# Kernel optimization log

Hardware: AMD Instinct MI355X
Metric: run time of the kernel (lower is better)

The kernel has to match this reference:

```python
import jax, jax.numpy as jnp
import numpy as np

DIM = 64          # hidden dim
EDGE_DIM = 6      # edge feature dim
A = 6             # action_dim (torsion bins); also torsions per graph
B = 512           # num_graphs
NPG = 40          # nodes per graph
N = B * NPG       # 20480 nodes
E = 43008         # edges
T = B * A         # 3072 total torsions


def _lin_init(k, out_f, in_f):
    bound = 1.0 / np.sqrt(in_f)
    kw, kb = jax.random.split(k)
    w = jax.random.uniform(kw, (out_f, in_f), jnp.float32, -bound, bound)
    b = jax.random.uniform(kb, (out_f,), jnp.float32, -bound, bound)
    return w, b


def setup_inputs() -> dict:
    key = jax.random.key(0)
    ks = jax.random.split(key, 24)
    inp = {}
    inp['x'] = jax.random.normal(ks[0], (N, 3), jnp.float32)
    inp['edge_attr'] = jax.random.uniform(ks[1], (E, EDGE_DIM), jnp.float32)
    inp['edge_index'] = jax.random.randint(ks[2], (2, E), 0, N)
    inp['batch'] = jnp.arange(N, dtype=jnp.int32) // NPG            # graph-sorted
    inp['nrbidx'] = jnp.repeat(jnp.arange(B, dtype=jnp.int32), A)   # torsion -> graph
    inp['nonring'] = jax.random.randint(ks[3], (T, 4), 0, N)        # 4 atoms per torsion
    # parameters
    inp['lin0_w'], inp['lin0_b'] = _lin_init(ks[4], DIM, 3)
    inp['enn1_w'], inp['enn1_b'] = _lin_init(ks[5], DIM, EDGE_DIM)
    inp['enn2_w'], inp['enn2_b'] = _lin_init(ks[6], DIM * DIM, DIM)
    inp['root_w'] = jax.random.uniform(ks[7], (DIM, DIM), jnp.float32, -1/np.sqrt(DIM), 1/np.sqrt(DIM))
    inp['conv_b'] = jnp.zeros((DIM,), jnp.float32)
    inp['gru_w_ih'], inp['gru_b_ih'] = _lin_init(ks[8], 3 * DIM, DIM)
    inp['gru_w_hh'], inp['gru_b_hh'] = _lin_init(ks[9], 3 * DIM, DIM)
    inp['s2s_w_ih'], inp['s2s_b_ih'] = _lin_init(ks[10], 4 * DIM, 2 * DIM)
    inp['s2s_w_hh'], inp['s2s_b_hh'] = _lin_init(ks[11], 4 * DIM, DIM)
    inp['mem_w_ih'], inp['mem_b_ih'] = _lin_init(ks[12], 4 * DIM, 2 * DIM)
    inp['mem_w_hh'], inp['mem_b_hh'] = _lin_init(ks[13], 4 * DIM, DIM)
    inp['lin1_w'], inp['lin1_b'] = _lin_init(ks[14], DIM, 5 * DIM)
    inp['lin2_w'], inp['lin2_b'] = _lin_init(ks[15], A, DIM)
    return inp


def _lstm_cell(xin, hc, w_ih, w_hh, b_ih, b_hh):
    h, c = hc
    g = xin @ w_ih.T + b_ih + h @ w_hh.T + b_hh
    i, f, gg, o = jnp.split(g, 4, axis=-1)
    c2 = jax.nn.sigmoid(f) * c + jax.nn.sigmoid(i) * jnp.tanh(gg)
    h2 = jax.nn.sigmoid(o) * jnp.tanh(c2)
    return h2, (h2, c2)


def reference(x, edge_attr, lin0_w, lin0_b, enn1_w, enn1_b, enn2_w, enn2_b,
              root_w, conv_b, gru_w_ih, gru_b_ih, gru_w_hh, gru_b_hh,
              s2s_w_ih, s2s_b_ih, s2s_w_hh, s2s_b_hh,
              mem_w_ih, mem_b_ih, mem_w_hh, mem_b_hh,
              lin1_w, lin1_b, lin2_w, lin2_b,
              edge_index, batch, nrbidx, nonring):
    dim = DIM
    out = jax.nn.relu(x @ lin0_w.T + lin0_b)                         # (N, dim)
    # edge-conditioned weights (constant across the 6 iterations)
    ew = jax.nn.relu(edge_attr @ enn1_w.T + enn1_b)
    W = (ew @ enn2_w.T + enn2_b).reshape(-1, dim, dim)               # (E, dim, dim)
    src, dst = edge_index[0], edge_index[1]
    deg = jax.ops.segment_sum(jnp.ones_like(src, jnp.float32), dst, num_segments=N)
    denom = jnp.maximum(deg, 1.0)[:, None]
    h = out                                                          # GRU hidden
    for _ in range(6):
        msg = jnp.einsum('ei,eio->eo', out[src], W)                  # gather + bmm
        agg = jax.ops.segment_sum(msg, dst, num_segments=N) / denom  # scatter-mean
        m = jax.nn.relu(agg + out @ root_w + conv_b)                 # NNConv out
        gi = m @ gru_w_ih.T + gru_b_ih
        gh = h @ gru_w_hh.T + gru_b_hh
        ir, iz, inn = jnp.split(gi, 3, axis=-1)
        hr, hz, hn = jnp.split(gh, 3, axis=-1)
        r = jax.nn.sigmoid(ir + hr)
        z = jax.nn.sigmoid(iz + hz)
        n = jnp.tanh(inn + r * hn)
        h = (1.0 - z) * n + z * h
        out = h
    # Set2Set pooling (processing_steps=6)
    q_star = jnp.zeros((B, 2 * dim), out.dtype)
    hc = (jnp.zeros((B, dim), out.dtype), jnp.zeros((B, dim), out.dtype))
    for _ in range(6):
        q, hc = _lstm_cell(q_star, hc, s2s_w_ih, s2s_w_hh, s2s_b_ih, s2s_b_hh)
        e = jnp.sum(out * q[batch], axis=-1)                         # (N,)
        emax = jax.ops.segment_max(e, batch, num_segments=B)
        a = jnp.exp(e - emax[batch])
        a = a / jax.ops.segment_sum(a, batch, num_segments=B)[batch]
        r = jax.ops.segment_sum(a[:, None] * out, batch, num_segments=B)
        q_star = jnp.concatenate([q, r], axis=-1)                    # (B, 2*dim)
    # memory LSTM, one step, zero initial state
    hc0 = (jnp.zeros((B, dim), out.dtype), jnp.zeros((B, dim), out.dtype))
    lstm_out, (hx, cx) = _lstm_cell(q_star, hc0, mem_w_ih, mem_w_hh, mem_b_ih, mem_b_hh)
    t = lstm_out[nrbidx].reshape(B, 1, A, dim)
    nd = out[nonring.reshape(-1)].reshape(B, 4, A, dim)
    z2 = jnp.concatenate([t, nd], axis=1)                            # (B, 5, A, dim)
    z2 = jnp.transpose(z2, (0, 3, 2, 1)).reshape(-1, 5 * dim)        # (T, 5*dim)
    z2 = jax.nn.relu(z2 @ lin1_w.T + lin1_b)
    z2 = z2 @ lin2_w.T + lin2_b                                      # (T, A)
    logit = z2.reshape(B, A, A)   # equal torsion counts -> pad_sequence == reshape
    return (logit, hx[None], cx[None])
```

## Files before the change

kernel.cpp:

```cpp
#include <hip/hip_runtime.h>
#include <hip/hip_fp16.h>

#define NN 20480
#define EE 43008
#define BB 512
#define TT 3072

typedef _Float16 f16;
typedef _Float16 f16x8 __attribute__((ext_vector_type(8)));
typedef float f32x4 __attribute__((ext_vector_type(4)));

__device__ __forceinline__ float sigm(float x) { return 1.0f / (1.0f + __expf(-x)); }
__device__ __forceinline__ float tanh_f(float x) {
    float xc = fminf(fmaxf(x, -15.f), 15.f);
    float t = __expf(2.f * xc);
    return (t - 1.f) / (t + 1.f);
}

__global__ void k_prep0(const float* __restrict__ x, const float* __restrict__ ea,
                        const float* __restrict__ l0w, const float* __restrict__ l0b,
                        const float* __restrict__ e1w, const float* __restrict__ e1b,
                        const float* __restrict__ e2w, const float* __restrict__ e2b,
                        const float* __restrict__ rootw,
                        const float* __restrict__ gwih, const float* __restrict__ gwhh,
                        const float* __restrict__ swih, const float* __restrict__ swhh,
                        const float* __restrict__ mwih,
                        float* __restrict__ feat, f16* __restrict__ feat16, f16* __restrict__ ew16,
                        f16* __restrict__ qmtp, float* __restrict__ deg,
                        f16* __restrict__ rootp, f16* __restrict__ wihp, f16* __restrict__ whhp,
                        float* __restrict__ s2sihT, float* __restrict__ s2shhT,
                        float* __restrict__ memihT)
{
    const int S0 = NN;
    const int S1 = S0 + NN * 64;
    const int S2 = S1 + EE * 64;
    const int S3 = S2 + 130 * 256 * 8;
    const int S4 = S3 + 4096;
    const int S5 = S4 + 12288;
    const int S6 = S5 + 12288;
    const int S7 = S6 + 128 * 256;
    const int S8 = S7 + 64 * 256;
    const int S9 = S8 + 128 * 256;
    for (int idx = blockIdx.x * blockDim.x + threadIdx.x; idx < S9; idx += gridDim.x * blockDim.x) {
        if (idx < S0) {
            deg[idx] = 0.f;
        } else if (idx < S1) {
            int t = idx - S0; int n = t >> 6, o = t & 63;
            float v = l0b[o] + x[n * 3] * l0w[o * 3] + x[n * 3 + 1] * l0w[o * 3 + 1] + x[n * 3 + 2] * l0w[o * 3 + 2];
            v = fmaxf(v, 0.f);
            feat[t] = v; feat16[t] = (f16)v;
        } else if (idx < S2) {
            int t = idx - S1; int e = t >> 6, o = t & 63;
            float acc = e1b[o];
#pragma unroll
            for (int j = 0; j < 6; ++j) acc += ea[e * 6 + j] * e1w[o * 6 + j];
            ew16[t] = (f16)fmaxf(acc, 0.f);
        } else if (idx < S3) {
            int t = idx - S2;
            int j = t & 7;
            int lane = (t >> 3) & 63;
            int cc = t >> 9;
            int c = cc >> 2, ct = cc & 3;
            int n = (ct << 4) | (lane & 15);
            int col = c * 32 + ((lane >> 4) << 3) + j;
            float v;
            if (col < 4096) v = e2w[(((col >> 6) << 6) + n) * 64 + (col & 63)];
            else            v = e2b[(col - 4096) * 64 + n];
            qmtp[t] = (f16)v;
        } else if (idx < S4) {
            int t = idx - S3; int j = t & 7; int lane = (t >> 3) & 63;
            int cc = t >> 9;
            int ct = cc >> 1, c = cc & 1;
            int n = ct * 16 + (lane & 15);
            int k = c * 32 + ((lane >> 4) << 3) + j;
            rootp[t] = (f16)rootw[k * 64 + n];
        } else if (idx < S5) {
            int t = idx - S4; int j = t & 7; int lane = (t >> 3) & 63;
            int cc = t >> 9;
            int gct = cc >> 1, c = cc & 1;
            int g = gct * 16 + (lane & 15);
            int k = c * 32 + ((lane >> 4) << 3) + j;
            wihp[t] = (f16)gwih[g * 64 + k];
        } else if (idx < S6) {
            int t = idx - S5; int j = t & 7; int lane = (t >> 3) & 63;
            int cc = t >> 9;
            int gct = cc >> 1, c = cc & 1;
            int g = gct * 16 + (lane & 15);
            int k = c * 32 + ((lane >> 4) << 3) + j;
            whhp[t] = (f16)gwhh[g * 64 + k];
        }
        else if (idx < S7)   { int t = idx - S6; int k = t >> 8, j = t & 255; s2sihT[t] = swih[j * 128 + k]; }
        else if (idx < S8)   { int t = idx - S7; int k = t >> 8, j = t & 255; s2shhT[t] = swhh[j * 64 + k]; }
        else                 { int t = idx - S8; int k = t >> 8, j = t & 255; memihT[t] = mwih[j * 128 + k]; }
    }
}

__global__ void k_prep1(const int* __restrict__ dstp, float* __restrict__ deg)
{
    int e = blockIdx.x * blockDim.x + threadIdx.x;
    if (e < EE) atomicAdd(&deg[dstp[e]], 1.0f);
}

__global__ __launch_bounds__(1024) void k_scan(const float* __restrict__ deg,
                                               int* __restrict__ rowptr, int* __restrict__ fill)
{
    __shared__ int part[1024];
    const int t = threadIdx.x;
    const int base = t * 20;
    int local[20];
    int s = 0;
#pragma unroll
    for (int j = 0; j < 20; ++j) { local[j] = s; s += (int)deg[base + j]; }
    part[t] = s;
    __syncthreads();
    for (int off = 1; off < 1024; off <<= 1) {
        int u = (t >= off) ? part[t - off] : 0;
        __syncthreads();
        part[t] += u;
        __syncthreads();
    }
    const int coff = part[t] - s;
#pragma unroll
    for (int j = 0; j < 20; ++j) { rowptr[base + j] = coff + local[j]; fill[base + j] = 0; }
    if (t == 1023) rowptr[NN] = part[1023];
}

__global__ void k_fill(const int* __restrict__ dstp, const int* __restrict__ rowptr,
                       int* __restrict__ fill, int* __restrict__ eidx)
{
    int e = blockIdx.x * blockDim.x + threadIdx.x;
    if (e < EE) {
        int d = dstp[e];
        int slot = atomicAdd(&fill[d], 1);
        eidx[rowptr[d] + slot] = e;
    }
}

__global__ __launch_bounds__(256, 3) void k_msg(const f16* __restrict__ feat16, const f16* __restrict__ ew16,
                                                const f16* __restrict__ qmtp,
                                                const int* __restrict__ srcp,
                                                float* __restrict__ msg)
{
    __shared__ f16 s_lds[64 * 64];
    __shared__ f16 w_lds[64 * 64];
    __shared__ float cmb[2][64][36];
    const int tid = threadIdx.x;
    const int e0 = blockIdx.x * 64;
    {
        int row = tid >> 2, q = tid & 3;
        int sn = srcp[e0 + row];
        const uint4* gs = (const uint4*)(feat16 + (size_t)sn * 64 + q * 16);
        const uint4* gw = (const uint4*)(ew16 + (size_t)(e0 + row) * 64 + q * 16);
        uint4 s0v = gs[0], s1v = gs[1];
        uint4 w0v = gw[0], w1v = gw[1];
        char* sbw = (char*)s_lds;
        char* wbw = (char*)w_lds;
        int swz = (row & 7) << 4;
        *(uint4*)(sbw + row * 128 + ((q * 32) ^ swz)) = s0v;
        *(uint4*)(sbw + row * 128 + ((q * 32 + 16) ^ swz)) = s1v;
        *(uint4*)(wbw + row * 128 + ((q * 32) ^ swz)) = w0v;
        *(uint4*)(wbw + row * 128 + ((q * 32 + 16) ^ swz)) = w1v;
    }
    __syncthreads();
    const int wv = tid >> 6, l = tid & 63;
    const int lh = l >> 4, ll = l & 15;
    const int cp = wv & 1;
    const int kp = wv >> 1;
    const int ctb = cp * 2;
    const char* sb = (const char*)s_lds;
    const char* wb = (const char*)w_lds;
    int rowv[4], swzv[4];
#pragma unroll
    for (int rg = 0; rg < 4; ++rg) { rowv[rg] = rg * 16 + ll; swzv[rg] = (rowv[rg] & 7) << 4; }
    f16x8 wf[4][2];
#pragma unroll
    for (int rg = 0; rg < 4; ++rg) {
        wf[rg][0] = *(const f16x8*)(wb + rowv[rg] * 128 + ((lh * 16) ^ swzv[rg]));
        wf[rg][1] = *(const f16x8*)(wb + rowv[rg] * 128 + ((64 + lh * 16) ^ swzv[rg]));
    }
    const f16x8* base = (const f16x8*)qmtp + l;
    f32x4 acc[4][2] = {};
    const int i0 = kp * 32;
    f16x8 S[3][2][2];
#pragma unroll
    for (int pp = 0; pp < 3; ++pp)
#pragma unroll
        for (int ab = 0; ab < 2; ++ab)
#pragma unroll
            for (int j = 0; j < 2; ++j)
                S[pp][ab][j] = base[((2 * (i0 + pp) + ab) * 4 + ctb + j) * 64];
    f16x8 sc[4];
#pragma unroll
    for (int p = 0; p < 32; ++p) {
        if ((p & 7) == 0) {
#pragma unroll
            for (int rg = 0; rg < 4; ++rg)
                sc[rg] = *(const f16x8*)(sb + rowv[rg] * 128 + ((((i0 + p) * 2)) ^ swzv[rg]));
        }
        const int bi = p % 3;
        __builtin_amdgcn_s_setprio(1);
#pragma unroll
        for (int rg = 0; rg < 4; ++rg) {
            f16 s = sc[rg][p & 7];
            f16x8 a0, a1;
#pragma unroll
            for (int j8 = 0; j8 < 8; ++j8) { a0[j8] = wf[rg][0][j8] * s; a1[j8] = wf[rg][1][j8] * s; }
#pragma unroll
            for (int j = 0; j < 2; ++j) {
                acc[rg][j] = __builtin_amdgcn_mfma_f32_16x16x32_f16(a0, S[bi][0][j], acc[rg][j], 0, 0, 0);
                acc[rg][j] = __builtin_amdgcn_mfma_f32_16x16x32_f16(a1, S[bi][1][j], acc[rg][j], 0, 0, 0);
            }
        }
        __builtin_amdgcn_s_setprio(0);
        int inext = i0 + p + 3; if (inext > 64) inext = 64;
#pragma unroll
        for (int ab = 0; ab < 2; ++ab)
#pragma unroll
            for (int j = 0; j < 2; ++j)
                S[bi][ab][j] = base[((2 * inext + ab) * 4 + ctb + j) * 64];
    }
    if (kp == 1) {
#pragma unroll
        for (int rg = 0; rg < 4; ++rg) {
            f16x8 sf0 = *(const f16x8*)(sb + rowv[rg] * 128 + ((lh * 16) ^ swzv[rg]));
            f16x8 sf1 = *(const f16x8*)(sb + rowv[rg] * 128 + ((64 + lh * 16) ^ swzv[rg]));
#pragma unroll
            for (int j = 0; j < 2; ++j) {
                acc[rg][j] = __builtin_amdgcn_mfma_f32_16x16x32_f16(sf0, S[2][0][j], acc[rg][j], 0, 0, 0);
                acc[rg][j] = __builtin_amdgcn_mfma_f32_16x16x32_f16(sf1, S[2][1][j], acc[rg][j], 0, 0, 0);
            }
        }
#pragma unroll
        for (int rg = 0; rg < 4; ++rg)
#pragma unroll
            for (int j = 0; j < 2; ++j)
#pragma unroll
                for (int q = 0; q < 4; ++q)
                    cmb[cp][rg * 16 + lh * 4 + q][j * 16 + ll] = acc[rg][j][q];
    }
    __syncthreads();
    if (kp == 0) {
#pragma unroll
        for (int rg = 0; rg < 4; ++rg)
#pragma unroll
            for (int q = 0; q < 4; ++q) {
                int r = rg * 16 + lh * 4 + q;
#pragma unroll
                for (int j = 0; j < 2; ++j) {
                    float v = acc[rg][j][q] + cmb[cp][r][j * 16 + ll];
                    msg[(size_t)(e0 + r) * 64 + ctb * 16 + j * 16 + ll] = v;
                }
            }
    }
}

__global__ __launch_bounds__(256) void k_node(float* __restrict__ feat, f16* __restrict__ feat16,
        const float* __restrict__ msg, const int* __restrict__ rowptr,
        const int* __restrict__ eidx, const float* __restrict__ deg,
        const f16* __restrict__ rootp, const f16* __restrict__ wihp, const f16* __restrict__ whhp,
        const float* __restrict__ conv_b, const float* __restrict__ bih, const float* __restrict__ bhh)
{
    __shared__ f16 h16[16 * 64];
    __shared__ f16 m16[16 * 64];
    __shared__ float aggm[16][68];
    const int tid = threadIdx.x;
    const int wv = tid >> 6, l = tid & 63;
    const int lh = l >> 4, ll = l & 15;
    const int nb = blockIdx.x * 16;
    char* hb = (char*)h16;
    char* mb = (char*)m16;
#pragma unroll
    for (int i = 0; i < 4; ++i) {
        int nd = wv * 4 + i;
        int n = nb + nd;
        float hv = feat[(size_t)n * 64 + l];
        int r0 = rowptr[n], r1 = rowptr[n + 1];
        float a = 0.f;
        for (int r = r0; r < r1; ++r) a += msg[(size_t)eidx[r] * 64 + l];
        aggm[nd][l] = a;
        int swz = (nd & 7) << 4;
        *(f16*)(hb + nd * 128 + ((l * 2) ^ swz)) = (f16)hv;
    }
    __syncthreads();
    const int rsw = (ll & 7) << 4;
    f16x8 hA0 = *(const f16x8*)(hb + ll * 128 + ((lh * 16) ^ rsw));
    f16x8 hA1 = *(const f16x8*)(hb + ll * 128 + ((64 + lh * 16) ^ rsw));
    const int col = wv * 16 + ll;
    float invd[4];
#pragma unroll
    for (int q = 0; q < 4; ++q) invd[q] = 1.0f / fmaxf(deg[nb + lh * 4 + q], 1.0f);
    {
        f16x8 b0 = *(const f16x8*)(rootp + ((size_t)(wv * 2 + 0) * 64 + l) * 8);
        f16x8 b1 = *(const f16x8*)(rootp + ((size_t)(wv * 2 + 1) * 64 + l) * 8);
        f32x4 acc = {};
        acc = __builtin_amdgcn_mfma_f32_16x16x32_f16(hA0, b0, acc, 0, 0, 0);
        acc = __builtin_amdgcn_mfma_f32_16x16x32_f16(hA1, b1, acc, 0, 0, 0);
        float cb = conv_b[col];
#pragma unroll
        for (int q = 0; q < 4; ++q) {
            int row = lh * 4 + q;
            float mv = fmaxf(aggm[row][col] * invd[q] + acc[q] + cb, 0.f);
            int swz = (row & 7) << 4;
            *(f16*)(mb + row * 128 + ((col * 2) ^ swz)) = (f16)mv;
        }
    }
    __syncthreads();
    f16x8 mA0 = *(const f16x8*)(mb + ll * 128 + ((lh * 16) ^ rsw));
    f16x8 mA1 = *(const f16x8*)(mb + ll * 128 + ((64 + lh * 16) ^ rsw));
    f32x4 gi0 = {}, gi1 = {}, gi2 = {}, gh0 = {}, gh1 = {}, gh2 = {};
    {
        f16x8 b;
        b = *(const f16x8*)(wihp + ((size_t)((wv + 0) * 2 + 0) * 64 + l) * 8);
        gi0 = __builtin_amdgcn_mfma_f32_16x16x32_f16(mA0, b, gi0, 0, 0, 0);
        b = *(const f16x8*)(wihp + ((size_t)((wv + 0) * 2 + 1) * 64 + l) * 8);
        gi0 = __builtin_amdgcn_mfma_f32_16x16x32_f16(mA1, b, gi0, 0, 0, 0);
        b = *(const f16x8*)(wihp + ((size_t)((wv + 4) * 2 + 0) * 64 + l) * 8);
        gi1 = __builtin_amdgcn_mfma_f32_16x16x32_f16(mA0, b, gi1, 0, 0, 0);
        b = *(const f16x8*)(wihp + ((size_t)((wv + 4) * 2 + 1) * 64 + l) * 8);
        gi1 = __builtin_amdgcn_mfma_f32_16x16x32_f16(mA1, b, gi1, 0, 0, 0);
        b = *(const f16x8*)(wihp + ((size_t)((wv + 8) * 2 + 0) * 64 + l) * 8);
        gi2 = __builtin_amdgcn_mfma_f32_16x16x32_f16(mA0, b, gi2, 0, 0, 0);
        b = *(const f16x8*)(wihp + ((size_t)((wv + 8) * 2 + 1) * 64 + l) * 8);
        gi2 = __builtin_amdgcn_mfma_f32_16x16x32_f16(mA1, b, gi2, 0, 0, 0);
        b = *(const f16x8*)(whhp + ((size_t)((wv + 0) * 2 + 0) * 64 + l) * 8);
        gh0 = __builtin_amdgcn_mfma_f32_16x16x32_f16(hA0, b, gh0, 0, 0, 0);
        b = *(const f16x8*)(whhp + ((size_t)((wv + 0) * 2 + 1) * 64 + l) * 8);
        gh0 = __builtin_amdgcn_mfma_f32_16x16x32_f16(hA1, b, gh0, 0, 0, 0);
        b = *(const f16x8*)(whhp + ((size_t)((wv + 4) * 2 + 0) * 64 + l) * 8);
        gh1 = __builtin_amdgcn_mfma_f32_16x16x32_f16(hA0, b, gh1, 0, 0, 0);
        b = *(const f16x8*)(whhp + ((size_t)((wv + 4) * 2 + 1) * 64 + l) * 8);
        gh1 = __builtin_amdgcn_mfma_f32_16x16x32_f16(hA1, b, gh1, 0, 0, 0);
        b = *(const f16x8*)(whhp + ((size_t)((wv + 8) * 2 + 0) * 64 + l) * 8);
        gh2 = __builtin_amdgcn_mfma_f32_16x16x32_f16(hA0, b, gh2, 0, 0, 0);
        b = *(const f16x8*)(whhp + ((size_t)((wv + 8) * 2 + 1) * 64 + l) * 8);
        gh2 = __builtin_amdgcn_mfma_f32_16x16x32_f16(hA1, b, gh2, 0, 0, 0);
    }
    {
        float bi0 = bih[col], bi1 = bih[64 + col], bi2 = bih[128 + col];
        float bh0 = bhh[col], bh1 = bhh[64 + col], bh2 = bhh[128 + col];
#pragma unroll
        for (int q = 0; q < 4; ++q) {
            int n = nb + lh * 4 + q;
            float r = sigm(gi0[q] + bi0 + gh0[q] + bh0);
            float z = sigm(gi1[q] + bi1 + gh1[q] + bh1);
            float nn2 = tanh_f(gi2[q] + bi2 + r * (gh2[q] + bh2));
            float hold = feat[(size_t)n * 64 + col];
            float hn = (1.f - z) * nn2 + z * hold;
            feat[(size_t)n * 64 + col] = hn;
            feat16[(size_t)n * 64 + col] = (f16)hn;
        }
    }
}

__global__ __launch_bounds__(512) void k_s2s(const float* __restrict__ feat,
                                             const float* __restrict__ s2sihT, const float* __restrict__ s2shhT,
                                             const float* __restrict__ sbih, const float* __restrict__ sbhh,
                                             const float* __restrict__ memihT,
                                             const float* __restrict__ mbih, const float* __restrict__ mbhh,
                                             float* __restrict__ lstm_out, float* __restrict__ dout)
{
    __shared__ float ft[2][64][49];
    __shared__ float qs[2][128];
    __shared__ float hh[2][64];
    __shared__ float cc[2][64];
    __shared__ float qv[2][64];
    __shared__ float g0p[2][256];
    __shared__ float g1p[2][256];
    const int t = threadIdx.x;
    const int g0 = blockIdx.x * 2;
    for (int i = t; i < 2 * 40 * 64; i += 512) {
        int g = i / 2560;
        int rem = i - g * 2560;
        int row = rem >> 6, o = rem & 63;
        ft[g][o][row] = feat[((size_t)(g0 + g) * 40 + row) * 64 + o];
    }
    if (t < 256) qs[t >> 7][t & 127] = 0.f;
    if (t < 128) { hh[t >> 6][t & 63] = 0.f; cc[t >> 6][t & 63] = 0.f; }
    __syncthreads();
    const int jj = t & 255;
    const int half = t >> 8;
    const int gg = t >> 6, gl = t & 63;
    const float b_s = sbih[jj] + sbhh[jj];
    const float b_m = mbih[jj] + mbhh[jj];
    for (int step = 0; step < 7; ++step) {
        const bool mem = (step == 6);
        {
            float a0, a1;
            if (!mem) {
                if (half == 0) {
                    a0 = b_s; a1 = b_s;
#pragma unroll 16
                    for (int k = 0; k < 96; ++k) {
                        float w = s2sihT[k * 256 + jj];
                        a0 += qs[0][k] * w;
                        a1 += qs[1][k] * w;
                    }
                } else {
                    a0 = 0.f; a1 = 0.f;
#pragma unroll 16
                    for (int k = 96; k < 128; ++k) {
                        float w = s2sihT[k * 256 + jj];
                        a0 += qs[0][k] * w;
                        a1 += qs[1][k] * w;
                    }
#pragma unroll 16
                    for (int k = 0; k < 64; ++k) {
                        float w = s2shhT[k * 256 + jj];
                        a0 += hh[0][k] * w;
                        a1 += hh[1][k] * w;
                    }
                }
            } else {
                if (half == 0) {
                    a0 = b_m; a1 = b_m;
#pragma unroll 16
                    for (int k = 0; k < 64; ++k) {
                        float w = memihT[k * 256 + jj];
                        a0 += qs[0][k] * w;
                        a1 += qs[1][k] * w;
                    }
                } else {
                    a0 = 0.f; a1 = 0.f;
#pragma unroll 16
                    for (int k = 64; k < 128; ++k) {
                        float w = memihT[k * 256 + jj];
                        a0 += qs[0][k] * w;
                        a1 += qs[1][k] * w;
                    }
                }
            }
            if (half == 0) { g0p[0][jj] = a0; g0p[1][jj] = a1; }
            else           { g1p[0][jj] = a0; g1p[1][jj] = a1; }
        }
        __syncthreads();
        if (t < 128) {
            float ii = sigm(g0p[gg][gl]        + g1p[gg][gl]);
            float ff = sigm(g0p[gg][64 + gl]   + g1p[gg][64 + gl]);
            float g2 = tanh_f(g0p[gg][128 + gl] + g1p[gg][128 + gl]);
            float oo = sigm(g0p[gg][192 + gl]  + g1p[gg][192 + gl]);
            float cprev = mem ? 0.f : cc[gg][gl];
            float c2 = ff * cprev + ii * g2;
            float h2 = oo * tanh_f(c2);
            if (!mem) {
                cc[gg][gl] = c2; hh[gg][gl] = h2;
                qv[gg][gl] = h2; qs[gg][gl] = h2;
                const int g = gg, l = gl;
                float e = -1e30f;
                if (l < 40) {
                    float s = 0.f;
                    for (int o = 0; o < 64; ++o) s += ft[g][o][l] * qv[g][o];
                    e = s;
                }
                float emax = e;
#pragma unroll
                for (int off = 32; off; off >>= 1) emax = fmaxf(emax, __shfl_xor(emax, off));
                float av = (l < 40) ? __expf(e - emax) : 0.f;
                float asum = av;
#pragma unroll
                for (int off = 32; off; off >>= 1) asum += __shfl_xor(asum, off);
                av /= asum;
                float r = 0.f;
                for (int nd = 0; nd < 40; ++nd) r += __shfl(av, nd) * ft[g][l][nd];
                qs[g][64 + l] = r;
            } else {
                int gidx = g0 + gg;
                lstm_out[(size_t)gidx * 64 + gl] = h2;
                dout[18432 + (size_t)gidx * 64 + gl] = h2;
                dout[18432 + 32768 + (size_t)gidx * 64 + gl] = c2;
            }
        }
        __syncthreads();
    }
}

__global__ __launch_bounds__(256) void k_final(const float* __restrict__ feat,
                                               const float* __restrict__ lstm_out,
                                               const int* __restrict__ nrbidx, const int* __restrict__ nonring,
                                               const float* __restrict__ l1w, const float* __restrict__ l1b,
                                               const float* __restrict__ l2w, const float* __restrict__ l2b,
                                               float* __restrict__ dout)
{
    __shared__ float z_lds[4][320];
    __shared__ float y_lds[4][64];
    const int wv = threadIdx.x >> 6, l = threadIdx.x & 63;
    const int r = blockIdx.x * 4 + wv;
    const int b = r / 6, rr = r - b * 6;
#pragma unroll
    for (int p = 0; p < 5; ++p) {
        int c = p * 64 + l;
        int f2 = rr * 320 + c;
        int d = f2 / 30;
        int rem = f2 - d * 30;
        int a = rem / 5;
        int s = rem - a * 5;
        float v;
        if (s == 0) v = lstm_out[(size_t)nrbidx[b * 6 + a] * 64 + d];
        else {
            int atom = nonring[b * 24 + (s - 1) * 6 + a];
            v = feat[(size_t)atom * 64 + d];
        }
        z_lds[wv][c] = v;
    }
    __syncthreads();
    {
        float acc = l1b[l];
        const float4* wr = (const float4*)(l1w + (size_t)l * 320);
        const float4* zr = (const float4*)(z_lds[wv]);
        for (int c4 = 0; c4 < 80; ++c4) {
            float4 w4 = wr[c4]; float4 z4 = zr[c4];
            acc += w4.x * z4.x + w4.y * z4.y + w4.z * z4.z + w4.w * z4.w;
        }
        y_lds[wv][l] = fmaxf(acc, 0.f);
    }
    __syncthreads();
    if (l < 6) {
        float acc = l2b[l];
        const float* yr = y_lds[wv];
        const float* w2 = l2w + l * 64;
        for (int o = 0; o < 64; ++o) acc += yr[o] * w2[o];
        dout[b * 36 + rr * 6 + l] = acc;
    }
}

extern "C" void kernel_launch(void* const* d_in, const int* in_sizes, int n_in,
                              void* d_out, int out_size, void* d_ws, size_t ws_size,
                              hipStream_t stream)
{
    const float* x    = (const float*)d_in[0];
    const float* ea   = (const float*)d_in[1];
    const int*   ei   = (const int*)d_in[2];
    const int*   nrb  = (const int*)d_in[4];
    const int*   nonr = (const int*)d_in[5];
    const float* l0w  = (const float*)d_in[6];  const float* l0b = (const float*)d_in[7];
    const float* e1w  = (const float*)d_in[8];  const float* e1b = (const float*)d_in[9];
    const float* e2w  = (const float*)d_in[10]; const float* e2b = (const float*)d_in[11];
    const float* rootw= (const float*)d_in[12]; const float* convb = (const float*)d_in[13];
    const float* gwih = (const float*)d_in[14]; const float* gbih = (const float*)d_in[15];
    const float* gwhh = (const float*)d_in[16]; const float* gbhh = (const float*)d_in[17];
    const float* swih = (const float*)d_in[18]; const float* sbih = (const float*)d_in[19];
    const float* swhh = (const float*)d_in[20]; const float* sbhh = (const float*)d_in[21];
    const float* mwih = (const float*)d_in[22]; const float* mbih = (const float*)d_in[23];
    const float* mbhh = (const float*)d_in[25];
    const float* l1w  = (const float*)d_in[26]; const float* l1b = (const float*)d_in[27];
    const float* l2w  = (const float*)d_in[28]; const float* l2b = (const float*)d_in[29];
    const int* srcp = ei;
    const int* dstp = ei + EE;
    float* dout = (float*)d_out;

    char* w = (char*)d_ws;
    size_t off = 0;
    auto alloc = [&](size_t bytes) -> void* {
        off = (off + 255) & ~(size_t)255;
        void* p = w + off;
        off += bytes;
        return p;
    };
    float* feat    = (float*)alloc((size_t)NN * 64 * 4);
    f16*   feat16  = (f16*)alloc((size_t)NN * 64 * 2);
    f16*   ew16    = (f16*)alloc((size_t)EE * 64 * 2);
    f16*   qmtp    = (f16*)alloc((size_t)132 * 256 * 8 * 2);
    float* msg     = (float*)alloc((size_t)EE * 64 * 4);
    float* deg     = (float*)alloc((size_t)NN * 4);
    int*   rowptr  = (int*)alloc((size_t)(NN + 1) * 4);
    int*   fill    = (int*)alloc((size_t)NN * 4);
    int*   eidx    = (int*)alloc((size_t)EE * 4);
    f16*   rootp   = (f16*)alloc((size_t)4096 * 2);
    f16*   wihp    = (f16*)alloc((size_t)12288 * 2);
    f16*   whhp    = (f16*)alloc((size_t)12288 * 2);
    float* s2sihT  = (float*)alloc((size_t)128 * 256 * 4);
    float* s2shhT  = (float*)alloc((size_t)64 * 256 * 4);
    float* memihT  = (float*)alloc((size_t)128 * 256 * 4);
    float* lstmo   = (float*)alloc((size_t)BB * 64 * 4);
    (void)ws_size; (void)in_sizes; (void)n_in; (void)out_size;

    hipLaunchKernelGGL(k_prep0, dim3(1024), dim3(256), 0, stream,
                       x, ea, l0w, l0b, e1w, e1b, e2w, e2b, rootw, gwih, gwhh, swih, swhh, mwih,
                       feat, feat16, ew16, qmtp, deg, rootp, wihp, whhp, s2sihT, s2shhT, memihT);
    hipLaunchKernelGGL(k_prep1, dim3(EE / 256), dim3(256), 0, stream, dstp, deg);
    hipLaunchKernelGGL(k_scan, dim3(1), dim3(1024), 0, stream, deg, rowptr, fill);
    hipLaunchKernelGGL(k_fill, dim3(EE / 256), dim3(256), 0, stream, dstp, rowptr, fill, eidx);
    for (int it = 0; it < 6; ++it) {
        hipLaunchKernelGGL(k_msg, dim3(EE / 64), dim3(256), 0, stream,
                           feat16, ew16, qmtp, srcp, msg);
        hipLaunchKernelGGL(k_node, dim3(NN / 16), dim3(256), 0, stream,
                           feat, feat16, msg, rowptr, eidx, deg, rootp, wihp, whhp, convb, gbih, gbhh);
    }
    hipLaunchKernelGGL(k_s2s, dim3(BB / 2), dim3(512), 0, stream,
                       feat, s2sihT, s2shhT, sbih, sbhh, memihT, mbih, mbhh, lstmo, dout);
    hipLaunchKernelGGL(k_final, dim3(TT / 4), dim3(256), 0, stream,
                       feat, lstmo, nrb, nonr, l1w, l1b, l2w, l2b, dout);
}
```

Baseline: 361.7 us.

## Split k_msg reduction four ways across waves, each wave covering all columns

Reworks the per-edge message kernel so each of the four waves owns a quarter of the 64-wide reduction dimension and computes all four 16-column output tiles, instead of the old split of two column halves by two K halves. Partial sums from three waves are combined through an enlarged LDS buffer and wave 0 writes the result. Each wave now holds twice the accumulators and issues all B-operand loads, which raises register pressure, so launch bounds drop from 3 to 2 waves per SIMD. The B-tile prefetch becomes a double buffer, and the qmtp buffer is enlarged to cover the extra prefetch rows read past the end.

```diff
diff --git a/kernel.cpp b/kernel.cpp
--- a/kernel.cpp
+++ b/kernel.cpp
@@ -136,14 +136,14 @@
     }
 }
 
-__global__ __launch_bounds__(256, 3) void k_msg(const f16* __restrict__ feat16, const f16* __restrict__ ew16,
+__global__ __launch_bounds__(256, 2) void k_msg(const f16* __restrict__ feat16, const f16* __restrict__ ew16,
                                                 const f16* __restrict__ qmtp,
                                                 const int* __restrict__ srcp,
                                                 float* __restrict__ msg)
 {
     __shared__ f16 s_lds[64 * 64];
     __shared__ f16 w_lds[64 * 64];
-    __shared__ float cmb[2][64][36];
+    __shared__ float cmb[3][64][68];
     const int tid = threadIdx.x;
     const int e0 = blockIdx.x * 64;
     {
@@ -162,11 +162,8 @@
         *(uint4*)(wbw + row * 128 + ((q * 32 + 16) ^ swz)) = w1v;
     }
     __syncthreads();
-    const int wv = tid >> 6, l = tid & 63;
+    const int kp = tid >> 6, l = tid & 63;
     const int lh = l >> 4, ll = l & 15;
-    const int cp = wv & 1;
-    const int kp = wv >> 1;
-    const int ctb = cp * 2;
     const char* sb = (const char*)s_lds;
     const char* wb = (const char*)w_lds;
     int rowv[4], swzv[4];
@@ -178,65 +175,80 @@
         wf[rg][0] = *(const f16x8*)(wb + rowv[rg] * 128 + ((lh * 16) ^ swzv[rg]));
         wf[rg][1] = *(const f16x8*)(wb + rowv[rg] * 128 + ((64 + lh * 16) ^ swzv[rg]));
     }
+    const int i0 = kp * 16;
+    f16x8 sc0[4], sc1[4];
+#pragma unroll
+    for (int rg = 0; rg < 4; ++rg) {
+        sc0[rg] = *(const f16x8*)(sb + rowv[rg] * 128 + ((i0 * 2) ^ swzv[rg]));
+        sc1[rg] = *(const f16x8*)(sb + rowv[rg] * 128 + ((i0 * 2 + 16) ^ swzv[rg]));
+    }
     const f16x8* base = (const f16x8*)qmtp + l;
-    f32x4 acc[4][2] = {};
-    const int i0 = kp * 32;
-    f16x8 S[3][2][2];
-#pragma unroll
-    for (int pp = 0; pp < 3; ++pp)
+    f32x4 acc[4][4] = {};
+    f16x8 SA[8], SB[8];
+    auto issue = [&](f16x8 (&S)[8], int i) {
 #pragma unroll
         for (int ab = 0; ab < 2; ++ab)
 #pragma unroll
-            for (int j = 0; j < 2; ++j)
-                S[pp][ab][j] = base[((2 * (i0 + pp) + ab) * 4 + ctb + j) * 64];
-    f16x8 sc[4];
-#pragma unroll
-    for (int p = 0; p < 32; ++p) {
-        if ((p & 7) == 0) {
-#pragma unroll
-            for (int rg = 0; rg < 4; ++rg)
-                sc[rg] = *(const f16x8*)(sb + rowv[rg] * 128 + ((((i0 + p) * 2)) ^ swzv[rg]));
-        }
-        const int bi = p % 3;
+            for (int ct = 0; ct < 4; ++ct)
+                S[ab * 4 + ct] = base[((2 * i + ab) * 4 + ct) * 64];
+    };
+    issue(SA, i0);
+    issue(SB, i0 + 1);
+#pragma unroll
+    for (int pp = 0; pp < 16; pp += 2) {
         __builtin_amdgcn_s_setprio(1);
 #pragma unroll
         for (int rg = 0; rg < 4; ++rg) {
-            f16 s = sc[rg][p & 7];
+            f16 s = (pp < 8) ? sc0[rg][pp] : sc1[rg][pp - 8];
             f16x8 a0, a1;
 #pragma unroll
             for (int j8 = 0; j8 < 8; ++j8) { a0[j8] = wf[rg][0][j8] * s; a1[j8] = wf[rg][1][j8] * s; }
 #pragma unroll
-            for (int j = 0; j < 2; ++j) {
-                acc[rg][j] = __builtin_amdgcn_mfma_f32_16x16x32_f16(a0, S[bi][0][j], acc[rg][j], 0, 0, 0);
-                acc[rg][j] = __builtin_amdgcn_mfma_f32_16x16x32_f16(a1, S[bi][1][j], acc[rg][j], 0, 0, 0);
+            for (int ct = 0; ct < 4; ++ct) {
+                acc[rg][ct] = __builtin_amdgcn_mfma_f32_16x16x32_f16(a0, SA[ct], acc[rg][ct], 0, 0, 0);
+                acc[rg][ct] = __builtin_amdgcn_mfma_f32_16x16x32_f16(a1, SA[4 + ct], acc[rg][ct], 0, 0, 0);
             }
         }
         __builtin_amdgcn_s_setprio(0);
-        int inext = i0 + p + 3; if (inext > 64) inext = 64;
-#pragma unroll
-        for (int ab = 0; ab < 2; ++ab)
-#pragma unroll
-            for (int j = 0; j < 2; ++j)
-                S[bi][ab][j] = base[((2 * inext + ab) * 4 + ctb + j) * 64];
-    }
-    if (kp == 1) {
+        issue(SA, i0 + pp + 2);
+        __builtin_amdgcn_s_setprio(1);
+#pragma unroll
+        for (int rg = 0; rg < 4; ++rg) {
+            f16 s = (pp + 1 < 8) ? sc0[rg][pp + 1] : sc1[rg][pp + 1 - 8];
+            f16x8 a0, a1;
+#pragma unroll
+            for (int j8 = 0; j8 < 8; ++j8) { a0[j8] = wf[rg][0][j8] * s; a1[j8] = wf[rg][1][j8] * s; }
+#pragma unroll
+            for (int ct = 0; ct < 4; ++ct) {
+                acc[rg][ct] = __builtin_amdgcn_mfma_f32_16x16x32_f16(a0, SB[ct], acc[rg][ct], 0, 0, 0);
+                acc[rg][ct] = __builtin_amdgcn_mfma_f32_16x16x32_f16(a1, SB[4 + ct], acc[rg][ct], 0, 0, 0);
+            }
+        }
+        __builtin_amdgcn_s_setprio(0);
+        issue(SB, i0 + pp + 3);
+    }
+    if (kp == 3) {
+        f16x8 BBf[8];
+        issue(BBf, 64);
 #pragma unroll
         for (int rg = 0; rg < 4; ++rg) {
             f16x8 sf0 = *(const f16x8*)(sb + rowv[rg] * 128 + ((lh * 16) ^ swzv[rg]));
             f16x8 sf1 = *(const f16x8*)(sb + rowv[rg] * 128 + ((64 + lh * 16) ^ swzv[rg]));
 #pragma unroll
-            for (int j = 0; j < 2; ++j) {
-                acc[rg][j] = __builtin_amdgcn_mfma_f32_16x16x32_f16(sf0, S[2][0][j], acc[rg][j], 0, 0, 0);
-                acc[rg][j] = __builtin_amdgcn_mfma_f32_16x16x32_f16(sf1, S[2][1][j], acc[rg][j], 0, 0, 0);
+            for (int ct = 0; ct < 4; ++ct) {
+                acc[rg][ct] = __builtin_amdgcn_mfma_f32_16x16x32_f16(sf0, BBf[ct], acc[rg][ct], 0, 0, 0);
+                acc[rg][ct] = __builtin_amdgcn_mfma_f32_16x16x32_f16(sf1, BBf[4 + ct], acc[rg][ct], 0, 0, 0);
             }
         }
+    }
+    if (kp > 0) {
 #pragma unroll
         for (int rg = 0; rg < 4; ++rg)
 #pragma unroll
-            for (int j = 0; j < 2; ++j)
+            for (int ct = 0; ct < 4; ++ct)
 #pragma unroll
                 for (int q = 0; q < 4; ++q)
-                    cmb[cp][rg * 16 + lh * 4 + q][j * 16 + ll] = acc[rg][j][q];
+                    cmb[kp - 1][rg * 16 + lh * 4 + q][ct * 16 + ll] = acc[rg][ct][q];
     }
     __syncthreads();
     if (kp == 0) {
@@ -246,9 +258,10 @@
             for (int q = 0; q < 4; ++q) {
                 int r = rg * 16 + lh * 4 + q;
 #pragma unroll
-                for (int j = 0; j < 2; ++j) {
-                    float v = acc[rg][j][q] + cmb[cp][r][j * 16 + ll];
-                    msg[(size_t)(e0 + r) * 64 + ctb * 16 + j * 16 + ll] = v;
+                for (int ct = 0; ct < 4; ++ct) {
+                    int c = ct * 16 + ll;
+                    float v = acc[rg][ct][q] + cmb[0][r][c] + cmb[1][r][c] + cmb[2][r][c];
+                    msg[(size_t)(e0 + r) * 64 + c] = v;
                 }
             }
     }
@@ -558,7 +571,7 @@
     float* feat    = (float*)alloc((size_t)NN * 64 * 4);
     f16*   feat16  = (f16*)alloc((size_t)NN * 64 * 2);
     f16*   ew16    = (f16*)alloc((size_t)EE * 64 * 2);
-    f16*   qmtp    = (f16*)alloc((size_t)132 * 256 * 8 * 2);
+    f16*   qmtp    = (f16*)alloc((size_t)136 * 256 * 8 * 2);
     float* msg     = (float*)alloc((size_t)EE * 64 * 4);
     float* deg     = (float*)alloc((size_t)NN * 4);
     int*   rowptr  = (int*)alloc((size_t)(NN + 1) * 4);
```

Result: no change. 368.3 us (+1.8%).

## Permute edges into destination-sorted order and stagger weight-slice traversal per block

Applied to the files above, without the earlier changes.

Adds a one-time permutation kernel that reorders the per-edge weight features and source indices into CSR (destination-sorted) order. The message kernel then writes messages in that order, so the node aggregation reads contiguous rows instead of gathering through eidx. The message kernel also rotates its starting k-slice by block index so concurrent blocks read different parts of the shared weight tensor, spreading cache/channel pressure. Costs an extra edge-feature buffer, a prep pass, and a slightly larger qmtp allocation.

```diff
diff --git a/kernel.cpp b/kernel.cpp
--- a/kernel.cpp
+++ b/kernel.cpp
@@ -136,9 +136,21 @@
     }
 }
 
-__global__ __launch_bounds__(256, 3) void k_msg(const f16* __restrict__ feat16, const f16* __restrict__ ew16,
+__global__ void k_perm(const int* __restrict__ eidx, const int* __restrict__ srcp,
+                       int* __restrict__ sp, const f16* __restrict__ ew16, f16* __restrict__ ewp)
+{
+    int idx = blockIdx.x * 256 + threadIdx.x;
+    if (idx < EE * 64) {
+        int r = idx >> 6, c = idx & 63;
+        int e = eidx[r];
+        ewp[idx] = ew16[((size_t)e << 6) + c];
+        if (c == 0) sp[r] = srcp[e];
+    }
+}
+
+__global__ __launch_bounds__(256, 3) void k_msg(const f16* __restrict__ feat16, const f16* __restrict__ ewp,
                                                 const f16* __restrict__ qmtp,
-                                                const int* __restrict__ srcp,
+                                                const int* __restrict__ sp,
                                                 float* __restrict__ msg)
 {
     __shared__ f16 s_lds[64 * 64];
@@ -148,9 +160,9 @@
     const int e0 = blockIdx.x * 64;
     {
         int row = tid >> 2, q = tid & 3;
-        int sn = srcp[e0 + row];
+        int sn = sp[e0 + row];
         const uint4* gs = (const uint4*)(feat16 + (size_t)sn * 64 + q * 16);
-        const uint4* gw = (const uint4*)(ew16 + (size_t)(e0 + row) * 64 + q * 16);
+        const uint4* gw = (const uint4*)(ewp + (size_t)(e0 + row) * 64 + q * 16);
         uint4 s0v = gs[0], s1v = gs[1];
         uint4 w0v = gw[0], w1v = gw[1];
         char* sbw = (char*)s_lds;
@@ -167,6 +179,7 @@
     const int cp = wv & 1;
     const int kp = wv >> 1;
     const int ctb = cp * 2;
+    const int rot = (blockIdx.x & 3) << 3;
     const char* sb = (const char*)s_lds;
     const char* wb = (const char*)w_lds;
     int rowv[4], swzv[4];
@@ -183,19 +196,22 @@
     const int i0 = kp * 32;
     f16x8 S[3][2][2];
 #pragma unroll
-    for (int pp = 0; pp < 3; ++pp)
+    for (int pp = 0; pp < 3; ++pp) {
+        int ii = i0 + ((pp + rot) & 31);
 #pragma unroll
         for (int ab = 0; ab < 2; ++ab)
 #pragma unroll
             for (int j = 0; j < 2; ++j)
-                S[pp][ab][j] = base[((2 * (i0 + pp) + ab) * 4 + ctb + j) * 64];
+                S[pp][ab][j] = base[((2 * ii + ab) * 4 + ctb + j) * 64];
+    }
     f16x8 sc[4];
 #pragma unroll
     for (int p = 0; p < 32; ++p) {
+        int ii = i0 + ((p + rot) & 31);
         if ((p & 7) == 0) {
 #pragma unroll
             for (int rg = 0; rg < 4; ++rg)
-                sc[rg] = *(const f16x8*)(sb + rowv[rg] * 128 + ((((i0 + p) * 2)) ^ swzv[rg]));
+                sc[rg] = *(const f16x8*)(sb + rowv[rg] * 128 + ((ii * 2) ^ swzv[rg]));
         }
         const int bi = p % 3;
         __builtin_amdgcn_s_setprio(1);
@@ -212,7 +228,7 @@
             }
         }
         __builtin_amdgcn_s_setprio(0);
-        int inext = i0 + p + 3; if (inext > 64) inext = 64;
+        int inext = i0 + (((p + 3) + rot) & 31);
 #pragma unroll
         for (int ab = 0; ab < 2; ++ab)
 #pragma unroll
@@ -220,14 +236,20 @@
                 S[bi][ab][j] = base[((2 * inext + ab) * 4 + ctb + j) * 64];
     }
     if (kp == 1) {
+        f16x8 B0[2], B1[2];
+#pragma unroll
+        for (int j = 0; j < 2; ++j) {
+            B0[j] = base[((2 * 64 + 0) * 4 + ctb + j) * 64];
+            B1[j] = base[((2 * 64 + 1) * 4 + ctb + j) * 64];
+        }
 #pragma unroll
         for (int rg = 0; rg < 4; ++rg) {
             f16x8 sf0 = *(const f16x8*)(sb + rowv[rg] * 128 + ((lh * 16) ^ swzv[rg]));
             f16x8 sf1 = *(const f16x8*)(sb + rowv[rg] * 128 + ((64 + lh * 16) ^ swzv[rg]));
 #pragma unroll
             for (int j = 0; j < 2; ++j) {
-                acc[rg][j] = __builtin_amdgcn_mfma_f32_16x16x32_f16(sf0, S[2][0][j], acc[rg][j], 0, 0, 0);
-                acc[rg][j] = __builtin_amdgcn_mfma_f32_16x16x32_f16(sf1, S[2][1][j], acc[rg][j], 0, 0, 0);
+                acc[rg][j] = __builtin_amdgcn_mfma_f32_16x16x32_f16(sf0, B0[j], acc[rg][j], 0, 0, 0);
+                acc[rg][j] = __builtin_amdgcn_mfma_f32_16x16x32_f16(sf1, B1[j], acc[rg][j], 0, 0, 0);
             }
         }
 #pragma unroll
@@ -256,7 +278,7 @@
 
 __global__ __launch_bounds__(256) void k_node(float* __restrict__ feat, f16* __restrict__ feat16,
         const float* __restrict__ msg, const int* __restrict__ rowptr,
-        const int* __restrict__ eidx, const float* __restrict__ deg,
+        const float* __restrict__ deg,
         const f16* __restrict__ rootp, const f16* __restrict__ wihp, const f16* __restrict__ whhp,
         const float* __restrict__ conv_b, const float* __restrict__ bih, const float* __restrict__ bhh)
 {
@@ -276,7 +298,7 @@
         float hv = feat[(size_t)n * 64 + l];
         int r0 = rowptr[n], r1 = rowptr[n + 1];
         float a = 0.f;
-        for (int r = r0; r < r1; ++r) a += msg[(size_t)eidx[r] * 64 + l];
+        for (int r = r0; r < r1; ++r) a += msg[(size_t)r * 64 + l];
         aggm[nd][l] = a;
         int swz = (nd & 7) << 4;
         *(f16*)(hb + nd * 128 + ((l * 2) ^ swz)) = (f16)hv;
@@ -558,12 +580,14 @@
     float* feat    = (float*)alloc((size_t)NN * 64 * 4);
     f16*   feat16  = (f16*)alloc((size_t)NN * 64 * 2);
     f16*   ew16    = (f16*)alloc((size_t)EE * 64 * 2);
-    f16*   qmtp    = (f16*)alloc((size_t)132 * 256 * 8 * 2);
+    f16*   ewp     = (f16*)alloc((size_t)EE * 64 * 2);
+    f16*   qmtp    = (f16*)alloc((size_t)136 * 256 * 8 * 2);
     float* msg     = (float*)alloc((size_t)EE * 64 * 4);
     float* deg     = (float*)alloc((size_t)NN * 4);
     int*   rowptr  = (int*)alloc((size_t)(NN + 1) * 4);
     int*   fill    = (int*)alloc((size_t)NN * 4);
     int*   eidx    = (int*)alloc((size_t)EE * 4);
+    int*   sp      = (int*)alloc((size_t)EE * 4);
     f16*   rootp   = (f16*)alloc((size_t)4096 * 2);
     f16*   wihp    = (f16*)alloc((size_t)12288 * 2);
     f16*   whhp    = (f16*)alloc((size_t)12288 * 2);
@@ -579,11 +603,12 @@
     hipLaunchKernelGGL(k_prep1, dim3(EE / 256), dim3(256), 0, stream, dstp, deg);
     hipLaunchKernelGGL(k_scan, dim3(1), dim3(1024), 0, stream, deg, rowptr, fill);
     hipLaunchKernelGGL(k_fill, dim3(EE / 256), dim3(256), 0, stream, dstp, rowptr, fill, eidx);
+    hipLaunchKernelGGL(k_perm, dim3(EE * 64 / 256), dim3(256), 0, stream, eidx, srcp, sp, ew16, ewp);
     for (int it = 0; it < 6; ++it) {
         hipLaunchKernelGGL(k_msg, dim3(EE / 64), dim3(256), 0, stream,
-                           feat16, ew16, qmtp, srcp, msg);
+                           feat16, ewp, qmtp, sp, msg);
         hipLaunchKernelGGL(k_node, dim3(NN / 16), dim3(256), 0, stream,
-                           feat, feat16, msg, rowptr, eidx, deg, rootp, wihp, whhp, convb, gbih, gbhh);
+                           feat, feat16, msg, rowptr, deg, rootp, wihp, whhp, convb, gbih, gbhh);
     }
     hipLaunchKernelGGL(k_s2s, dim3(BB / 2), dim3(512), 0, stream,
                        feat, s2sihT, s2shhT, sbih, sbhh, memihT, mbih, mbhh, lstmo, dout);
```

After: 340.9 us, median of 3. -5.8%, faster.
